# Kernel tuning notes

Hardware: AMD Instinct MI355X
Metric: run time of the kernel (lower is better)

## Reference

```python
import jax, jax.numpy as jnp
import numpy as np

EPS = 1e-15

def gcn_sparse(x, row, col, ew, W, b, n):
    # PyG GCNConv: h = x@W; add self-loops (weight 1); sym-normalize; aggregate at col (target); + bias
    h = x @ W
    loop = jnp.arange(n)
    r = jnp.concatenate([row, loop])
    c = jnp.concatenate([col, loop])
    w = jnp.concatenate([ew, jnp.ones((n,), x.dtype)])
    deg = jax.ops.segment_sum(w, c, num_segments=n)
    dinv = jnp.where(deg > 0, deg ** -0.5, 0.0)
    norm = dinv[r] * w * dinv[c]
    out = jax.ops.segment_sum(norm[:, None] * h[r], c, num_segments=n)
    return out + b

def gcn_dense(x, adj, W, b):
    # Dense equivalent of dense_to_sparse + GCNConv: existing nonzero self-loops keep their
    # weight, zero-diagonal nodes get a self-loop of weight 1 (add_remaining_self_loops).
    diag = jnp.diagonal(adj)
    adj_h = adj + jnp.diag(jnp.where(diag == 0, 1.0, 0.0).astype(adj.dtype))
    deg = adj_h.sum(axis=0)  # degree at target (col) nodes
    dinv = jnp.where(deg > 0, deg ** -0.5, 0.0)
    a_norm = dinv[:, None] * adj_h * dinv[None, :]  # norm_ij = d_i^-1/2 a_ij d_j^-1/2
    return a_norm.T @ (x @ W) + b  # out_j = sum_i norm_ij h_i

def diff_pool(x, adj, s, mask=None):
    s = jax.nn.softmax(s, axis=-1)
    if mask is not None:
        x = x * mask[:, None]
        s = s * mask[:, None]
    out = s.T @ x                      # [C, F]
    out_adj = s.T @ (adj @ s)          # [C, C]
    link = jnp.linalg.norm(adj - s @ s.T) / adj.size
    ent = jnp.mean(jnp.sum(-s * jnp.log(s + EPS), axis=-1))
    return out, out_adj, link, ent

def setup_inputs() -> dict:
    N, E, F, H, C1, C2, NC = 8192, 262144, 128, 128, 1024, 128, 16
    key = jax.random.key(0)
    ks = jax.random.split(key, 16)
    x0 = jax.random.normal(ks[0], (N, F), dtype=jnp.float32)
    edge_index = jax.random.randint(ks[1], (2, E), 0, N, dtype=jnp.int32)
    edge_weight = jax.random.uniform(ks[2], (E,), dtype=jnp.float32)
    adj = jnp.zeros((N, N), jnp.float32).at[edge_index[0], edge_index[1]].add(edge_weight)
    mask = jnp.ones((N,), jnp.float32)
    g = lambda k, i, o: jax.random.normal(k, (i, o), dtype=jnp.float32) * (1.0 / np.sqrt(i))
    return {
        'x0': x0, 'edge_index': edge_index, 'edge_weight': edge_weight,
        'adj': adj, 'mask': mask,
        'W0_in': g(ks[3], F, H),      'b0_in': jnp.zeros((H,)),
        'Wp1':   g(ks[4], H, C1),     'bp1':   jnp.zeros((C1,)),
        'W1_in': g(ks[5], H, H),      'b1_in': jnp.zeros((H,)),
        'Wp2':   g(ks[6], H, C2),     'bp2':   jnp.zeros((C2,)),
        'W2_in': g(ks[7], H, H),      'b2_in': jnp.zeros((H,)),
        'W1_out': g(ks[8], 2 * H, H), 'b1_out': jnp.zeros((H,)),
        'W0_out': g(ks[9], 2 * H, NC), 'b0_out': jnp.zeros((NC,)),
    }

def reference(x0, edge_index, edge_weight, adj, mask,
              W0_in, b0_in, Wp1, bp1, W1_in, b1_in, Wp2, bp2,
              W2_in, b2_in, W1_out, b1_out, W0_out, b0_out):
    n = x0.shape[0]
    row, col = edge_index[0], edge_index[1]
    x0_ = jax.nn.relu(gcn_sparse(x0, row, col, edge_weight, W0_in, b0_in, n))
    s1 = jax.nn.relu(gcn_sparse(x0_, row, col, edge_weight, Wp1, bp1, n))
    x1, adj1, l1, e1 = diff_pool(x0_, adj, s1, mask)
    x1_ = jax.nn.relu(gcn_dense(x1, adj1, W1_in, b1_in))
    s2 = jax.nn.relu(gcn_dense(x1_, adj1, Wp2, bp2))
    x2, adj2, l2, e2 = diff_pool(x1_, adj1, s2)
    x2_out = jax.nn.relu(gcn_dense(x2, adj2, W2_in, b2_in))
    x2_out_up = s2 @ x2_out  # unpool with pre-softmax relu s2, as in source
    x1_out = jax.nn.relu(gcn_dense(jnp.concatenate([x1_, x2_out_up], axis=1), adj1, W1_out, b1_out))
    x1_out_up = s1 @ x1_out
    x0_out = jax.nn.relu(gcn_sparse(jnp.concatenate([x0_, x1_out_up], axis=1), row, col, edge_weight, W0_out, b0_out, n))
    prediction = jax.nn.log_softmax(x0_out, axis=1)
    edge_loss = l1 + e1 + l2 + e2
    return prediction, s1, edge_loss, adj1
```

## Files before the change

### kernel.cpp

```cpp
#include <hip/hip_runtime.h>
#include <math.h>


#define N_NODES 8192
#define N_EDGES 262144

typedef __attribute__((ext_vector_type(8))) short short8;
typedef __attribute__((ext_vector_type(4))) float floatx4;

#define OFF_DEG     0
#define OFF_CNTC    8192
#define OFF_CNTR    16384
#define OFF_SCAL    24576
#define ZERO_FLOATS 24592
#define OFF_COLPTR  24592
#define OFF_ROWPTR  32785
#define OFF_CURC    40978
#define OFF_CURR    49170
#define OFF_COLR    57362
#define OFF_COLN    319506
#define OFF_ROWC    581650
#define OFF_ROWW    843794
#define OFF_DINV    1105938
#define OFF_X0      1114144
#define OFF_H0      2162720
#define OFF_S       3211296
#define OFF_AN1TB   OFF_S
#define OFF_ADJ1B   (OFF_S+524288)
#define OFF_HAT     (OFF_S+1048576)
#define OFF_HBT     (OFF_S+1114112)
#define OFF_HCATT   (OFF_S+1179648)
#define OFF_S2ST    (OFF_S+1245184)
#define OFF_X0T     7405600
#define OFF_X0B     7929888
#define A2          8454176
#define OFF_X1      (A2+0)
#define OFF_Y16     (A2+131072)
#define OFF_X1_     (A2+262144)
#define OFF_S2      (A2+524288)
#define OFF_S2S     (A2+655360)
#define OFF_U       (A2+786432)
#define OFF_X2      (A2+917504)
#define OFF_ADJ2    (A2+933888)
#define OFF_HC      (A2+950272)
#define OFF_X2_     (A2+966656)
#define OFF_Z2      (A2+999424)
#define OFF_P16     (A2+1392640)
#define OFF_DEG1    OFF_P16
#define OFF_DIAGV   (OFF_P16+1024)
#define OFF_DI2     (A2+1656832)
#define OFF_DF2     (A2+1656960)
#define OFF_ST      10111264
#define OFF_TBF     14305568
#define OFF_WP1T    OFF_TBF
#define OFF_PT      OFF_TBF
#define OFF_S1B     22694176
#define OFF_TT2     32131360

#define OUT_PRED 0
#define OUT_S1   131072
#define OUT_LOSS 8519680
#define OUT_ADJ1 8519681

__device__ __forceinline__ unsigned short f2bf(float f) {
    union { float f; unsigned u; } v; v.f = f;
    unsigned r = (v.u + 0x7FFF + ((v.u >> 16) & 1)) >> 16;
    return (unsigned short)r;
}
__device__ __forceinline__ float bf2f(unsigned short b) {
    union { unsigned u; float f; } v; v.u = (unsigned)b << 16; return v.f;
}
__device__ __forceinline__ void gl_lds16(const unsigned short* g, unsigned short* l) {
    __builtin_amdgcn_global_load_lds(
        (const __attribute__((address_space(1))) void*)g,
        (__attribute__((address_space(3))) void*)l, 16, 0, 0);
}


__global__ __launch_bounds__(256) void k_hist_gemm(
        const int* __restrict__ row, const int* __restrict__ col,
        const float* __restrict__ ew, int E,
        float* deg, int* cntc, int* cntr, float* sumA2,
        const float* __restrict__ A, const float* __restrict__ B,
        unsigned short* __restrict__ C) {
    __shared__ float As[16][68];
    __shared__ float Bs[16][68];
    int tid = threadIdx.x;
    if (blockIdx.x < 1024) {
        float* red = &As[0][0];
        int e = blockIdx.x * 256 + tid;
        float w2 = 0.f;
        if (e < E) {
            int r = row[e], c = col[e];
            float w = ew[e];
            atomicAdd(&deg[c], w);
            atomicAdd(&cntc[c], 1);
            atomicAdd(&cntr[r], 1);
            w2 = w * w;
        }
        red[tid] = w2; __syncthreads();
        for (int s = 128; s > 0; s >>= 1) { if (tid < s) red[tid] += red[tid + s]; __syncthreads(); }
        if (tid == 0) atomicAdd(sumA2, red[0]);
        return;
    }
    int bidx = blockIdx.x - 1024;
    int tx = tid & 15, ty = tid >> 4;
    int m0 = (bidx >> 1) * 64, n0 = (bidx & 1) * 64;
    const int M = 8192, N = 128, K = 128;
    float acc[4][4] = {};
    for (int k0 = 0; k0 < K; k0 += 16) {
        for (int l = 0; l < 4; ++l) {
            int idx = tid + 256 * l;
            int mm = idx >> 4, kk = idx & 15;
            As[kk][mm] = A[(size_t)(m0 + mm) * K + k0 + kk];
            int kk2 = idx >> 6, nn = idx & 63;
            Bs[kk2][nn] = B[(size_t)(k0 + kk2) * N + n0 + nn];
        }
        __syncthreads();
        #pragma unroll
        for (int kk = 0; kk < 16; ++kk) {
            float a[4], b[4];
            #pragma unroll
            for (int i = 0; i < 4; ++i) a[i] = As[kk][ty * 4 + i];
            #pragma unroll
            for (int j = 0; j < 4; ++j) b[j] = Bs[kk][tx * 4 + j];
            #pragma unroll
            for (int i = 0; i < 4; ++i)
                #pragma unroll
                for (int j = 0; j < 4; ++j) acc[i][j] += a[i] * b[j];
        }
        __syncthreads();
    }
    for (int i = 0; i < 4; ++i)
        for (int j = 0; j < 4; ++j)
            C[(size_t)(m0 + ty * 4 + i) * N + n0 + tx * 4 + j] = f2bf(acc[i][j]);
    (void)M;
}

__global__ __launch_bounds__(1024) void k_scan(const int* cntc, const int* cntr,
        int* colptr, int* rowptr, int* curc, int* curr, int n, int E,
        const float* __restrict__ deg, float* __restrict__ dinv) {
    __shared__ int part[1024];
    int tid = threadIdx.x;
    const int per = 8;
    for (int pass = 0; pass < 2; ++pass) {
        const int* cnt = pass ? cntr : cntc;
        int* ptr = pass ? rowptr : colptr;
        int* cur = pass ? curr : curc;
        int st = tid * per;
        int loc[per]; int s = 0;
        for (int i = 0; i < per; ++i) { loc[i] = s; s += cnt[st + i]; }
        part[tid] = s; __syncthreads();
        for (int off = 1; off < 1024; off <<= 1) {
            int v = part[tid];
            int add = (tid >= off) ? part[tid - off] : 0;
            __syncthreads();
            part[tid] = v + add;
            __syncthreads();
        }
        int pre = (tid == 0) ? 0 : part[tid - 1];
        for (int i = 0; i < per; ++i) { int v = pre + loc[i]; ptr[st + i] = v; cur[st + i] = v; }
        if (tid == 0) ptr[n] = E;
        __syncthreads();
    }
    for (int i = tid; i < n; i += 1024) {
        float d = deg[i] + 1.0f;
        dinv[i] = (d > 0.f) ? 1.0f / sqrtf(d) : 0.f;
    }
}

__global__ void k_scatter(const int* __restrict__ row, const int* __restrict__ col,
                          const float* __restrict__ ew, int E, const float* __restrict__ dinv,
                          int* curc, int* curr, int* colr, float* coln, int* rowc, float* roww) {
    int e = blockIdx.x * 256 + threadIdx.x;
    if (e >= E) return;
    int r = row[e], c = col[e];
    float w = ew[e];
    float nrm = dinv[r] * w * dinv[c];
    int p = atomicAdd(&curc[c], 1);
    colr[p] = r; coln[p] = nrm;
    int q = atomicAdd(&curr[r], 1);
    rowc[q] = c; roww[q] = w;
}


__global__ __launch_bounds__(256) void gemm_ab32(const float* __restrict__ A, const float* __restrict__ B,
        float* __restrict__ C, int M, int N, int K,
        const float* __restrict__ bias, int relu, int accum) {
    __shared__ float As[32][33];
    __shared__ float Bs[32][33];
    int tid = threadIdx.x, tx = tid & 15, ty = tid >> 4;
    int m0 = blockIdx.y * 32, n0 = blockIdx.x * 32;
    float acc[2][2] = {};
    for (int k0 = 0; k0 < K; k0 += 32) {
        #pragma unroll
        for (int l = 0; l < 4; ++l) {
            int idx = tid + 256 * l;
            int r = idx >> 5, c = idx & 31;
            As[r][c] = A[(size_t)(m0 + r) * K + k0 + c];
            Bs[r][c] = B[(size_t)(k0 + r) * N + n0 + c];
        }
        __syncthreads();
        #pragma unroll
        for (int kk = 0; kk < 32; ++kk) {
            float a0 = As[ty * 2][kk], a1 = As[ty * 2 + 1][kk];
            float b0 = Bs[kk][tx * 2], b1 = Bs[kk][tx * 2 + 1];
            acc[0][0] += a0 * b0; acc[0][1] += a0 * b1;
            acc[1][0] += a1 * b0; acc[1][1] += a1 * b1;
        }
        __syncthreads();
    }
    #pragma unroll
    for (int i = 0; i < 2; ++i)
        #pragma unroll
        for (int j = 0; j < 2; ++j) {
            int m = m0 + ty * 2 + i, n = n0 + tx * 2 + j;
            float v = acc[i][j];
            if (accum) v += C[(size_t)m * N + n];
            if (bias) v += bias[n];
// ... 7 lines not shown
    __shared__ float As[32][33];
    __shared__ float Bs[32][33];
    int tid = threadIdx.x, tx = tid & 15, ty = tid >> 4;
    int m0 = blockIdx.y * 32, n0 = blockIdx.x * 32;
    float acc[2][2] = {};
    for (int k0 = 0; k0 < K; k0 += 32) {
        #pragma unroll
        for (int l = 0; l < 4; ++l) {
            int idx = tid + 256 * l;
            int r = idx >> 5, c = idx & 31;
            As[r][c] = A[(size_t)(m0 + r) * K + k0 + c];
            Bs[r][c] = B[(size_t)(k0 + r) * N + n0 + c];
        }
        __syncthreads();
        #pragma unroll
        for (int kk = 0; kk < 32; ++kk) {
            float a0 = As[ty * 2][kk], a1 = As[ty * 2 + 1][kk];
            float b0 = Bs[kk][tx * 2], b1 = Bs[kk][tx * 2 + 1];
            acc[0][0] += a0 * b0; acc[0][1] += a0 * b1;
            acc[1][0] += a1 * b0; acc[1][1] += a1 * b1;
        }
        __syncthreads();
    }
    #pragma unroll
    for (int i = 0; i < 2; ++i)
        #pragma unroll
        for (int j = 0; j < 2; ++j)
            As[ty * 2 + i][tx * 2 + j] = acc[i][j];
    __syncthreads();
    int nl = tid >> 3, moff = (tid & 7) * 4;
    ushort4 o;
    o.x = f2bf(As[moff + 0][nl]);
    o.y = f2bf(As[moff + 1][nl]);
    o.z = f2bf(As[moff + 2][nl]);
    o.w = f2bf(As[moff + 3][nl]);
    *(ushort4*)(CT + (size_t)(n0 + nl) * M + m0 + moff) = o;
}

__global__ __launch_bounds__(256) void gemm_dual_bt(const float* __restrict__ A0,
        const float* __restrict__ B0, const float* __restrict__ A1, const float* __restrict__ B1,
        unsigned short* __restrict__ CT, int M, int N, int Kc) {
    __shared__ float As[32][33];
    __shared__ float Bs[32][33];
    int tid = threadIdx.x, tx = tid & 15, ty = tid >> 4;
    int m0 = blockIdx.y * 32, n0 = blockIdx.x * 32;
    float acc[2][2] = {};
    for (int src = 0; src < 2; ++src) {
        const float* A = src ? A1 : A0;
        const float* B = src ? B1 : B0;
        for (int k0 = 0; k0 < Kc; k0 += 32) {
            #pragma unroll
            for (int l = 0; l < 4; ++l) {
                int idx = tid + 256 * l;
                int r = idx >> 5, c = idx & 31;
                As[r][c] = A[(size_t)(m0 + r) * Kc + k0 + c];
                Bs[r][c] = B[(size_t)(k0 + r) * N + n0 + c];
            }
            __syncthreads();
            #pragma unroll
            for (int kk = 0; kk < 32; ++kk) {
                float a0 = As[ty * 2][kk], a1 = As[ty * 2 + 1][kk];
                float b0 = Bs[kk][tx * 2], b1 = Bs[kk][tx * 2 + 1];
                acc[0][0] += a0 * b0; acc[0][1] += a0 * b1;
                acc[1][0] += a1 * b0; acc[1][1] += a1 * b1;
            }
            __syncthreads();
        }
    }
    #pragma unroll
    for (int i = 0; i < 2; ++i)
        #pragma unroll
        for (int j = 0; j < 2; ++j)
            As[ty * 2 + i][tx * 2 + j] = acc[i][j];
    __syncthreads();
    int nl = tid >> 3, moff = (tid & 7) * 4;
    ushort4 o;
    o.x = f2bf(As[moff + 0][nl]);
    o.y = f2bf(As[moff + 1][nl]);
    o.z = f2bf(As[moff + 2][nl]);
    o.w = f2bf(As[moff + 3][nl]);
    *(ushort4*)(CT + (size_t)(n0 + nl) * M + m0 + moff) = o;
}

__global__ __launch_bounds__(256) void gemm_atb32n(const float* __restrict__ A, const float* __restrict__ B,
        float* __restrict__ C, int M, int N, int K,
        const float* __restrict__ bias, const float* __restrict__ kscale,
        const float* __restrict__ dfixv, const float* __restrict__ mscale) {
    __shared__ float As[32][33];
    __shared__ float Bs[32][33];
    int tid = threadIdx.x, tx = tid & 15, ty = tid >> 4;
    int m0 = blockIdx.y * 32, n0 = blockIdx.x * 32;
    float acc[2][2] = {};
    for (int k0 = 0; k0 < K; k0 += 32) {
        #pragma unroll
        for (int l = 0; l < 4; ++l) {
            int idx = tid + 256 * l;
            int r = idx >> 5, c = idx & 31;
            int k = k0 + r, m = m0 + c;
            float v = A[(size_t)k * M + m];
            if (k == m) v += dfixv[m];
            As[c][r] = v * kscale[k];
            Bs[r][c] = B[(size_t)k * N + n0 + c];
        }
        __syncthreads();
        #pragma unroll
        for (int kk = 0; kk < 32; ++kk) {
            float a0 = As[ty * 2][kk], a1 = As[ty * 2 + 1][kk];
            float b0 = Bs[kk][tx * 2], b1 = Bs[kk][tx * 2 + 1];
            acc[0][0] += a0 * b0; acc[0][1] += a0 * b1;
            acc[1][0] += a1 * b0; acc[1][1] += a1 * b1;
        }
        __syncthreads();
    }
    #pragma unroll
    for (int i = 0; i < 2; ++i)
        #pragma unroll
        for (int j = 0; j < 2; ++j) {
            int m = m0 + ty * 2 + i, n = n0 + tx * 2 + j;
            float v = acc[i][j] * mscale[m] + bias[n];
            C[(size_t)m * N + n] = fmaxf(v, 0.f);
        }
}

__global__ __launch_bounds__(256) void k_atb32_3(const float* __restrict__ A,
        const float* __restrict__ B0, const float* __restrict__ B1, const float* __restrict__ B2,
        float* __restrict__ C0, float* __restrict__ C1, float* ss_acc,
        int M, int N, int K) {
    __shared__ float As[32][33];
    __shared__ float Bs[32][33];
    __shared__ float red[256];
    int op = blockIdx.z;
    const float* B = (op == 0) ? B0 : (op == 1) ? B1 : B2;
    int tid = threadIdx.x, tx = tid & 15, ty = tid >> 4;
    int m0 = blockIdx.y * 32, n0 = blockIdx.x * 32;
    float acc[2][2] = {};
    for (int k0 = 0; k0 < K; k0 += 32) {
        #pragma unroll
        for (int l = 0; l < 4; ++l) {
            int idx = tid + 256 * l;
            int r = idx >> 5, c = idx & 31;
            As[c][r] = A[(size_t)(k0 + r) * M + m0 + c];
            Bs[r][c] = B[(size_t)(k0 + r) * N + n0 + c];
        }
        __syncthreads();
        #pragma unroll
        for (int kk = 0; kk < 32; ++kk) {
            float a0 = As[ty * 2][kk], a1 = As[ty * 2 + 1][kk];
            float b0 = Bs[kk][tx * 2], b1 = Bs[kk][tx * 2 + 1];
            acc[0][0] += a0 * b0; acc[0][1] += a0 * b1;
            acc[1][0] += a1 * b0; acc[1][1] += a1 * b1;
        }
        __syncthreads();
    }
    if (op == 2) {
        float ss = acc[0][0] * acc[0][0] + acc[0][1] * acc[0][1]
                 + acc[1][0] * acc[1][0] + acc[1][1] * acc[1][1];
        red[tid] = ss; __syncthreads();
        for (int s = 128; s > 0; s >>= 1) { if (tid < s) red[tid] += red[tid + s]; __syncthreads(); }
        if (tid == 0) atomicAdd(ss_acc, red[0]);
        return;
    }
    float* C = (op == 0) ? C0 : C1;
    #pragma unroll
    for (int i = 0; i < 2; ++i)
        #pragma unroll
        for (int j = 0; j < 2; ++j)
            C[(size_t)(m0 + ty * 2 + i) * N + n0 + tx * 2 + j] = acc[i][j];
}

__global__ __launch_bounds__(256) void k_hC_coldfix(
        const float* __restrict__ x2, const float* __restrict__ W2,
        float* __restrict__ hC, const float* __restrict__ adj2,
        float* di2, float* df2, float* cross2_out) {
    if (blockIdx.z == 0) {
        __shared__ float As[32][33];
        __shared__ float Bs[32][33];
        int tid = threadIdx.x, tx = tid & 15, ty = tid >> 4;
        int m0 = blockIdx.y * 32, n0 = blockIdx.x * 32;
        float acc[2][2] = {};
        for (int k0 = 0; k0 < 128; k0 += 32) {
            #pragma unroll
            for (int l = 0; l < 4; ++l) {
                int idx = tid + 256 * l;
                int r = idx >> 5, c = idx & 31;
                As[r][c] = x2[(size_t)(m0 + r) * 128 + k0 + c];
                Bs[r][c] = W2[(size_t)(k0 + r) * 128 + n0 + c];
            }
            __syncthreads();
            #pragma unroll
            for (int kk = 0; kk < 32; ++kk) {
                float a0 = As[ty * 2][kk], a1 = As[ty * 2 + 1][kk];
                float b0 = Bs[kk][tx * 2], b1 = Bs[kk][tx * 2 + 1];
                acc[0][0] += a0 * b0; acc[0][1] += a0 * b1;
                acc[1][0] += a1 * b0; acc[1][1] += a1 * b1;
            }
            __syncthreads();
        }
        #pragma unroll
        for (int i = 0; i < 2; ++i)
            #pragma unroll
            for (int j = 0; j < 2; ++j)
                hC[(size_t)(m0 + ty * 2 + i) * 128 + n0 + tx * 2 + j] = acc[i][j];
    } else {
        if (blockIdx.x | blockIdx.y) return;
        __shared__ float red[256];
        int tid = threadIdx.x;
        float diag = 0.f;
        if (tid < 128) {
            float s = 0.f;
            for (int i = 0; i < 128; ++i) s += adj2[(size_t)i * 128 + tid];
            diag = adj2[(size_t)tid * 128 + tid];
            float fix = (diag == 0.f) ? 1.0f : 0.f;
            s += fix;
            df2[tid] = fix;
            di2[tid] = (s > 0.f) ? 1.0f / sqrtf(s) : 0.f;
        }
        red[tid] = diag; __syncthreads();
        for (int st = 128; st > 0; st >>= 1) { if (tid < st) red[tid] += red[tid + st]; __syncthreads(); }
        if (tid == 0) *cross2_out = red[0];
    }
}


__global__ __launch_bounds__(256) void gemm_tn_bf16_tiles(
        const unsigned short* __restrict__ ST_,
        const unsigned short* __restrict__ TT_,
        const unsigned short* __restrict__ X0T_,
        float* __restrict__ P, int K) {
    __shared__ __align__(16) unsigned short As[128 * 64];
    __shared__ __align__(16) unsigned short Bs[128 * 64];
    int tid = threadIdx.x;
    int wave = tid >> 6, lane = tid & 63;
    int wm = wave >> 1, wn = wave & 1;
    int lin = blockIdx.x + gridDim.x * blockIdx.y;
    int p432 = (lin & 7) * 54 + (lin >> 3);
    int f = p432 >> 2, z = p432 & 3;
    int m = 0, Pfx = 0;
    while (f >= Pfx + 17 - m) { Pfx += 17 - m; ++m; }
    int r = f - Pfx;
    int t, n0; const unsigned short* B;
    if (r < 8)           { t = m * 8 + r;                                n0 = r * 128;    B = TT_; }
    else if (r < 16 - m) { int tj = m + (r - 8);
                           t = 64 + (8 * m - m * (m - 1) / 2) + (r - 8); n0 = tj * 128;   B = ST_; }
    else                 { t = 100 + m;                                  n0 = 0;          B = X0T_; }
    int m0 = m * 128;
    int kchunk = K >> 2;
    int k0 = z * kchunk;
    float* Pz = P + ((size_t)z * 108 + t) * 16384;
    floatx4 acc[4][4] = {};
    int q = lane >> 4, lm = lane & 15;
    int lrow = lane >> 3, lcol = (lane & 7) * 8;
    for (int kt = 0; kt < kchunk; kt += 64) {
        int gk0 = k0 + kt;
        #pragma unroll
        for (int p = 0; p < 4; ++p) {
            int rbase = wave * 32 + p * 8;
            int rrow = rbase + lrow;
            int scol = lcol ^ ((rrow & 7) * 8);
            gl_lds16(&ST_[(size_t)(m0 + rrow) * K + gk0 + scol], &As[rbase * 64]);
            gl_lds16(&B[(size_t)(n0 + rrow) * K + gk0 + scol], &Bs[rbase * 64]);
        }
        __syncthreads();
        #pragma unroll
        for (int ks = 0; ks < 64; ks += 32) {
            short8 af[4], bf[4];
            int kk = ks + q * 8;
            #pragma unroll
            for (int i = 0; i < 4; ++i) {
                int ml = wm * 64 + i * 16 + lm;
                af[i] = *(const short8*)(&As[ml * 64 + (kk ^ ((ml & 7) * 8))]);
                int nl = wn * 64 + i * 16 + lm;
                bf[i] = *(const short8*)(&Bs[nl * 64 + (kk ^ ((nl & 7) * 8))]);
            }
            #pragma unroll
            for (int i = 0; i < 4; ++i)
                #pragma unroll
                for (int j = 0; j < 4; ++j)
                    acc[i][j] = __builtin_amdgcn_mfma_f32_16x16x32_bf16(af[i], bf[j], acc[i][j], 0, 0, 0);
        }
        __syncthreads();
    }
    for (int i = 0; i < 4; ++i) {
        int lr = wm * 64 + i * 16 + q * 4;
        for (int j = 0; j < 4; ++j) {
            int lc = wn * 64 + j * 16 + lm;
            #pragma unroll
            for (int rr = 0; rr < 4; ++rr)
                Pz[(size_t)(lr + rr) * 128 + lc] = acc[i][j][rr];
        }
    }
}

__global__ __launch_bounds__(256) void k_reduce_tiles(
        const float* __restrict__ P,
        float* __restrict__ adj1o, unsigned short* __restrict__ adj1b,
        float* __restrict__ x1, float* __restrict__ deg1, float* __restrict__ diagv,
        float* __restrict__ scal) {
    __shared__ float colsum[128];
    __shared__ float red[256];
    int tile = blockIdx.y, half = blockIdx.x, tid = threadIdx.x;
    if (tid < 128) colsum[tid] = 0.f;
    __syncthreads();
    int m, n, kind;
// ... 187 lines not shown
    }
}

__global__ __launch_bounds__(256) void k_gemm16_mfma(
        const unsigned short* __restrict__ A0,
        const unsigned short* __restrict__ A1,
        const float* __restrict__ B0,
        const float* __restrict__ B1,
        float* __restrict__ C) {
    __shared__ __align__(16) unsigned short As[128 * 64];
    __shared__ __align__(16) unsigned short Bs[16 * 64];
    int tid = threadIdx.x, wave = tid >> 6, lane = tid & 63;
    int m0 = blockIdx.x * 128;
    int q = lane >> 4, lm = lane & 15;
    int lrow = lane >> 3, lcol = (lane & 7) * 8;
    floatx4 acc[2] = {};
    for (int seg = 0; seg < 2; ++seg) {
        const unsigned short* A = seg ? A1 : A0;
        const float* Bsrc = seg ? B1 : B0;
        int Ks = seg ? 1024 : 128;
        for (int kt = 0; kt < Ks; kt += 64) {
            #pragma unroll
            for (int p = 0; p < 4; ++p) {
                int rbase = wave * 32 + p * 8;
                int row = rbase + lrow;
                int scol = lcol ^ ((row & 7) * 8);
                gl_lds16(&A[(size_t)(m0 + row) * Ks + kt + scol], &As[rbase * 64]);
            }
            for (int e = tid; e < 1024; e += 256) {
                int n = e >> 6, kk = e & 63;
                Bs[n * 64 + (kk ^ ((n & 7) * 8))] = f2bf(Bsrc[(size_t)(kt + kk) * 16 + n]);
            }
            __syncthreads();
            #pragma unroll
            for (int ks = 0; ks < 64; ks += 32) {
                int kk = ks + q * 8;
                short8 bf = *(const short8*)(&Bs[lm * 64 + (kk ^ ((lm & 7) * 8))]);
                #pragma unroll
                for (int i = 0; i < 2; ++i) {
                    int ml = wave * 32 + i * 16 + lm;
                    short8 af = *(const short8*)(&As[ml * 64 + (kk ^ ((ml & 7) * 8))]);
                    acc[i] = __builtin_amdgcn_mfma_f32_16x16x32_bf16(af, bf, acc[i], 0, 0, 0);
                }
            }
            __syncthreads();
        }
    }
    #pragma unroll
    for (int i = 0; i < 2; ++i) {
        int rowb = m0 + wave * 32 + i * 16 + q * 4;
        #pragma unroll
        for (int r = 0; r < 4; ++r)
            C[(size_t)(rowb + r) * 16 + lm] = acc[i][r];
    }
}


__device__ __forceinline__ void f2b_body(float* tile ,
        const float* __restrict__ in, unsigned short* __restrict__ outb,
        int R, int C, const float* __restrict__ rowscale, int bx, int by, int t) {
    int rb = by * 64, cb = bx * 64;
    int lr = t >> 4, lc4 = (t & 15) * 4;
    #pragma unroll
    for (int p = 0; p < 4; ++p) {
        int r = rb + lr + p * 16;
        float4 v = *(const float4*)(in + (size_t)r * C + cb + lc4);
        float s = rowscale ? rowscale[r] : 1.0f;
        tile[(lr + p * 16) * 65 + lc4 + 0] = v.x * s;
        tile[(lr + p * 16) * 65 + lc4 + 1] = v.y * s;
        tile[(lr + p * 16) * 65 + lc4 + 2] = v.z * s;
        tile[(lr + p * 16) * 65 + lc4 + 3] = v.w * s;
    }
    __syncthreads();
    int cc0 = t >> 5, rr = (t & 31) * 2;
    #pragma unroll
    for (int p = 0; p < 8; ++p) {
        int cc = cc0 + p * 8;
        unsigned a = f2bf(tile[rr * 65 + cc]);
        unsigned b = f2bf(tile[(rr + 1) * 65 + cc]);
        *(unsigned*)(outb + (size_t)(cb + cc) * R + rb + rr) = a | (b << 16);
    }
}

__global__ __launch_bounds__(256) void k_f2b2(
        const float* __restrict__ in0, unsigned short* __restrict__ out0,
        const float* __restrict__ in1, unsigned short* __restrict__ out1,
        const float* __restrict__ mask) {
    __shared__ float tile[64 * 65];
    int b = blockIdx.x, t = threadIdx.x;
    if (b < 32) f2b_body(tile, in0, out0, 128, 1024, nullptr, b & 15, b >> 4, t);
    else { int bb = b - 32; f2b_body(tile, in1, out1, 8192, 128, mask, bb & 1, bb >> 1, t); }
}

__global__ __launch_bounds__(256) void k_transpose_b2b2(
        const unsigned short* __restrict__ in0, unsigned short* __restrict__ out0,
        const unsigned short* __restrict__ in1, unsigned short* __restrict__ out1,
        int R, int C) {
    __shared__ __align__(16) unsigned short tile[64][72];
    const unsigned short* in = blockIdx.z ? in1 : in0;
    unsigned short* out = blockIdx.z ? out1 : out0;
    int rb = blockIdx.y * 64, cb = blockIdx.x * 64;
    int t = threadIdx.x;
    int lr = t >> 3, lc = (t & 7) * 8;
    #pragma unroll
    for (int p = 0; p < 2; ++p) {
        int r = lr + p * 32;
        *(short8*)(&tile[r][lc]) = *(const short8*)(&in[(size_t)(rb + r) * C + cb + lc]);
    }
    __syncthreads();
    int cc0 = t >> 4, rr = (t & 15) * 4;
    #pragma unroll
    for (int p = 0; p < 4; ++p) {
        int cc = cc0 + p * 16;
        unsigned long long v = (unsigned long long)tile[rr][cc]
                             | ((unsigned long long)tile[rr + 1][cc] << 16)
                             | ((unsigned long long)tile[rr + 2][cc] << 32)
                             | ((unsigned long long)tile[rr + 3][cc] << 48);
        *(unsigned long long*)(&out[(size_t)(cb + cc) * R + rb + rr]) = v;
    }
}

__global__ __launch_bounds__(256) void k_anorm_hat(const float* __restrict__ adjm,
        const float* __restrict__ deg1, const float* __restrict__ diagv,
        unsigned short* __restrict__ outb,
        const float* __restrict__ Ax1, const float* __restrict__ BW1,
        unsigned short* __restrict__ HATo) {
    __shared__ float sm[64 * 65 + 192];
    int t = threadIdx.x;
    if (blockIdx.x < 256) {
        const int n = 1024;
        float* tile = sm;
        float* drow = sm + 4160;
        float* frow = sm + 4224;
        float* dcol = sm + 4288;
        int rb = (blockIdx.x >> 4) * 64, cb = (blockIdx.x & 15) * 64;
        if (t < 64) {
            int i = rb + t;
            float fi = (diagv[i] == 0.f) ? 1.0f : 0.f;
            float s = deg1[i] + fi;
            frow[t] = fi;
            drow[t] = (s > 0.f) ? 1.0f / sqrtf(s) : 0.f;
        } else if (t < 128) {
            int j = cb + (t - 64);
            float fj = (diagv[j] == 0.f) ? 1.0f : 0.f;
            float s = deg1[j] + fj;
            dcol[t - 64] = (s > 0.f) ? 1.0f / sqrtf(s) : 0.f;
        }
        __syncthreads();
        int lr = t >> 4, lc4 = (t & 15) * 4;
        #pragma unroll
        for (int p = 0; p < 4; ++p) {
            int rl = lr + p * 16;
            int i = rb + rl;
            float4 v = *(const float4*)(adjm + (size_t)i * n + cb + lc4);
            float di = drow[rl];
            float vv[4] = {v.x, v.y, v.z, v.w};
            #pragma unroll
            for (int qq = 0; qq < 4; ++qq) {
                int j = cb + lc4 + qq;
                float val = vv[qq];
                if (i == j) val += frow[rl];
                tile[rl * 65 + lc4 + qq] = di * val * dcol[lc4 + qq];
            }
        }
        __syncthreads();
        int cc0 = t >> 5, rr = (t & 31) * 2;
        #pragma unroll
        for (int p = 0; p < 8; ++p) {
            int cc = cc0 + p * 8;
            unsigned a = f2bf(tile[rr * 65 + cc]);
            unsigned b = f2bf(tile[(rr + 1) * 65 + cc]);
            *(unsigned*)(outb + (size_t)(cb + cc) * n + rb + rr) = a | (b << 16);
        }
        return;
// ... 205 lines not shown
    for (int q = 0; q < 8; ++q)
        ow[q] = (unsigned)f2bf(a[q * 2]) | ((unsigned)f2bf(a[q * 2 + 1]) << 16);
    uint4* outp = (uint4*)(tb + (size_t)r * 1024 + j0);
    outp[0] = make_uint4(ow[0], ow[1], ow[2], ow[3]);
    outp[1] = make_uint4(ow[4], ow[5], ow[6], ow[7]);
}


extern "C" void kernel_launch(void* const* d_in, const int* in_sizes, int n_in,
                              void* d_out, int out_size, void* d_ws, size_t ws_size,
                              hipStream_t stream) {
    const int N = N_NODES, E = N_EDGES;
    const float* x0     = (const float*)d_in[0];
    const int*   eidx   = (const int*)d_in[1];
    const float* ew     = (const float*)d_in[2];
    const float* mask   = (const float*)d_in[4];
    const float* W0_in  = (const float*)d_in[5];
    const float* b0_in  = (const float*)d_in[6];
    const float* Wp1    = (const float*)d_in[7];
    const float* bp1    = (const float*)d_in[8];
    const float* W1_in  = (const float*)d_in[9];
    const float* b1_in  = (const float*)d_in[10];
    const float* Wp2    = (const float*)d_in[11];
    const float* bp2    = (const float*)d_in[12];
    const float* W2_in  = (const float*)d_in[13];
    const float* b2_in  = (const float*)d_in[14];
    const float* W1_out = (const float*)d_in[15];
    const float* b1_out = (const float*)d_in[16];
    const float* W0_out = (const float*)d_in[17];
    const float* b0_out = (const float*)d_in[18];

    float* out   = (float*)d_out;
    float* predo = out + OUT_PRED;
    float* s1o   = out + OUT_S1;
    float* losso = out + OUT_LOSS;
    float* adj1o = out + OUT_ADJ1;

    float* wsf = (float*)d_ws;
    int*   wsi = (int*)d_ws;
    float* deg   = wsf + OFF_DEG;
    int*   cntc  = wsi + OFF_CNTC;
    int*   cntr  = wsi + OFF_CNTR;
    float* scal  = wsf + OFF_SCAL;
    int*   cptr  = wsi + OFF_COLPTR;
    int*   rptr  = wsi + OFF_ROWPTR;
    int*   curc  = wsi + OFF_CURC;
    int*   curr  = wsi + OFF_CURR;
    int*   colr  = wsi + OFF_COLR;
    float* coln  = wsf + OFF_COLN;
    int*   rowc  = wsi + OFF_ROWC;
    float* roww  = wsf + OFF_ROWW;
    float* dinv  = wsf + OFF_DINV;
    float* x0_   = wsf + OFF_X0;
    unsigned short* h0b   = (unsigned short*)(wsf + OFF_H0);
    unsigned short* Sb    = (unsigned short*)(wsf + OFF_S);
    unsigned short* TT    = (unsigned short*)(wsf + OFF_TT2);
    unsigned short* AN1TB = (unsigned short*)(wsf + OFF_AN1TB);
    unsigned short* ADJ1B = (unsigned short*)(wsf + OFF_ADJ1B);
    unsigned short* HAT   = (unsigned short*)(wsf + OFF_HAT);
    unsigned short* HBT   = (unsigned short*)(wsf + OFF_HBT);
    unsigned short* HCATT = (unsigned short*)(wsf + OFF_HCATT);
    unsigned short* S2ST  = (unsigned short*)(wsf + OFF_S2ST);
    unsigned short* ST    = (unsigned short*)(wsf + OFF_ST);
    unsigned short* TBF   = (unsigned short*)(wsf + OFF_TBF);
    unsigned short* WP1T  = (unsigned short*)(wsf + OFF_WP1T);
    unsigned short* X0T   = (unsigned short*)(wsf + OFF_X0T);
    unsigned short* x0b   = (unsigned short*)(wsf + OFF_X0B);
    unsigned short* s1b   = (unsigned short*)(wsf + OFF_S1B);
    float* PT    = wsf + OFF_PT;
    float* x1    = wsf + OFF_X1;
    float* y16   = wsf + OFF_Y16;
    float* x1_   = wsf + OFF_X1_;
    float* s2    = wsf + OFF_S2;
    float* S2s   = wsf + OFF_S2S;
    float* u     = wsf + OFF_U;
    float* x2    = wsf + OFF_X2;
    float* adj2  = wsf + OFF_ADJ2;
    float* hC    = wsf + OFF_HC;
    float* x2_   = wsf + OFF_X2_;
    float* z2    = wsf + OFF_Z2;
    float* p16   = wsf + OFF_P16;
    float* deg1  = wsf + OFF_DEG1;
    float* diagv = wsf + OFF_DIAGV;
    float* di2   = wsf + OFF_DI2;
    float* df2   = wsf + OFF_DF2;

    const int* row = eidx;
    const int* col = eidx + E;

    hipMemsetAsync(wsf, 0, (size_t)ZERO_FLOATS * sizeof(float), stream);
    hipMemsetAsync(deg1, 0, 1024 * sizeof(float), stream);
    hipMemsetAsync(y16, 0, 1024 * 16 * sizeof(float), stream);

    k_hist_gemm<<<1280, 256, 0, stream>>>(row, col, ew, E, deg, cntc, cntr, &scal[3],
                                          x0, W0_in, h0b);
    k_scan<<<1, 1024, 0, stream>>>(cntc, cntr, cptr, rptr, curc, curr, N, E, deg, dinv);
    k_scatter<<<E / 256, 256, 0, stream>>>(row, col, ew, E, dinv, curc, curr, colr, coln, rowc, roww);

    k_agg_b16<<<N, 64, 0, stream>>>(h0b, x0_, x0b, cptr, colr, coln, dinv, b0_in, 1);

    k_agg_b16<<<N, 64, 0, stream>>>(x0b, nullptr, h0b, cptr, colr, coln, dinv, nullptr, 0);
    k_f2b2<<<288, 256, 0, stream>>>(Wp1, WP1T, x0_, X0T, mask);
    gemm_tn_bf16_store<<<dim3(64, 8), 256, 0, stream>>>(h0b, WP1T, s1o, s1b, 8192, 1024, 128, bp1, 1);

    k_softmax1024<<<N, 256, 0, stream>>>(s1o, Sb, mask, &scal[0]);
    k_spmm_seg<<<N / 4, 256, 0, stream>>>(Sb, rptr, rowc, roww, TBF);
    k_transpose_b2b2<<<dim3(16, 128, 2), 256, 0, stream>>>(Sb, ST, TBF, TT, 8192, 1024);

    gemm_tn_bf16_tiles<<<dim3(108, 4), 256, 0, stream>>>(ST, TT, X0T, PT, 8192);
    k_reduce_tiles<<<dim3(2, 108), 256, 0, stream>>>(PT, adj1o, ADJ1B, x1, deg1, diagv, scal);
    k_anorm_hat<<<384, 256, 0, stream>>>(adj1o, deg1, diagv, AN1TB, x1, W1_in, HAT);

    gemm_tn_bf16_n128<<<dim3(16, 2), 256, 0, stream>>>(AN1TB, HAT, x1_, 1024, b1_in, 1, nullptr, nullptr);
    gemm_ab32_bt<<<dim3(4, 32), 256, 0, stream>>>(x1_, Wp2, HBT, 1024, 128, 128);
    gemm_tn_bf16_n128<<<dim3(16, 2), 256, 0, stream>>>(AN1TB, HBT, s2, 1024, bp2, 1, nullptr, nullptr);

    k_softmax128_t<<<1024, 128, 0, stream>>>(s2, S2s, S2ST, &scal[5]);
    gemm_tn_bf16_n128<<<dim3(16, 2), 256, 0, stream>>>(ADJ1B, S2ST, u, 1024, nullptr, 0, nullptr, nullptr);
    k_atb32_3<<<dim3(4, 4, 3), 256, 0, stream>>>(S2s, x1_, u, S2s, x2, adj2, &scal[7], 128, 128, 1024);

    k_hC_coldfix<<<dim3(4, 4, 2), 256, 0, stream>>>(x2, W2_in, hC, adj2, di2, df2, &scal[6]);
    gemm_atb32n<<<dim3(4, 4), 256, 0, stream>>>(adj2, hC, x2_, 128, 128, 128, b2_in, di2, df2, di2);

    gemm_ab32<<<dim3(4, 4), 256, 0, stream>>>(x2_, W1_out + 128 * 128, z2, 128, 128, 128, nullptr, 0, 0);
    gemm_dual_bt<<<dim3(4, 32), 256, 0, stream>>>(x1_, W1_out, s2, z2, HCATT, 1024, 128, 128);
    gemm_tn_bf16_n128<<<dim3(16, 2), 256, 0, stream>>>(AN1TB, HCATT, nullptr, 1024, b1_out, 1,
                                                       W0_out + 128 * 16, y16);

    k_gemm16_mfma<<<64, 256, 0, stream>>>(x0b, s1b, W0_out, y16, p16);
    k_agg16_ls<<<512, 256, 0, stream>>>(p16, predo, cptr, colr, coln, dinv, b0_out, scal, losso);
}
```

Baseline: 889.1 us.

## Fuse small pool-2 GEMMs and merge second aggregation with bf16 conversions

Rebuilds the second diff-pool stage's kernel chain. The u = adj1·S2 MFMA GEMM now runs alongside x2 and the S2ᵀS2 sum-of-squares in one launch. adj2 and hC share a second launch, and the adj2 column-degree/diag fix is computed redundantly per block inside the final normalized GEMM, removing one launch and the di2/df2 buffers. Separately, the second sparse aggregation is rewritten with 4 nodes per 256-thread block and 4-way edge unrolling, and it absorbs the Wp1/x0_ bf16 transpose-conversion kernel. The aim is fewer launches and better occupancy, at the cost of duplicated degree computation across 16 blocks.

```diff
diff --git a/kernel.cpp b/kernel.cpp
--- a/kernel.cpp
+++ b/kernel.cpp
@@ -48,8 +48,6 @@
 #define OFF_P16     (A2+1392640)
 #define OFF_DEG1    OFF_P16
 #define OFF_DIAGV   (OFF_P16+1024)
-#define OFF_DI2     (A2+1656832)
-#define OFF_DF2     (A2+1656960)
 #define OFF_ST      10111264
 #define OFF_TBF     14305568
 #define OFF_WP1T    OFF_TBF
@@ -106,7 +104,7 @@
     int bidx = blockIdx.x - 1024;
     int tx = tid & 15, ty = tid >> 4;
     int m0 = (bidx >> 1) * 64, n0 = (bidx & 1) * 64;
-    const int M = 8192, N = 128, K = 128;
+    const int N = 128, K = 128;
     float acc[4][4] = {};
     for (int k0 = 0; k0 < K; k0 += 16) {
         for (int l = 0; l < 4; ++l) {
@@ -134,7 +132,6 @@
     for (int i = 0; i < 4; ++i)
         for (int j = 0; j < 4; ++j)
             C[(size_t)(m0 + ty * 4 + i) * N + n0 + tx * 4 + j] = f2bf(acc[i][j]);
-    (void)M;
 }
 
 __global__ __launch_bounds__(1024) void k_scan(const int* cntc, const int* cntr,
@@ -308,31 +305,201 @@
     *(ushort4*)(CT + (size_t)(n0 + nl) * M + m0 + moff) = o;
 }
 
-__global__ __launch_bounds__(256) void gemm_atb32n(const float* __restrict__ A, const float* __restrict__ B,
-        float* __restrict__ C, int M, int N, int K,
-        const float* __restrict__ bias, const float* __restrict__ kscale,
-        const float* __restrict__ dfixv, const float* __restrict__ mscale) {
-    __shared__ float As[32][33];
-    __shared__ float Bs[32][33];
-    int tid = threadIdx.x, tx = tid & 15, ty = tid >> 4;
-    int m0 = blockIdx.y * 32, n0 = blockIdx.x * 32;
+__global__ __launch_bounds__(256) void k_u_x2(
+        const unsigned short* __restrict__ ADJ1B, const unsigned short* __restrict__ S2ST,
+        float* __restrict__ u,
+        const float* __restrict__ S2s, const float* __restrict__ x1_,
+        float* __restrict__ x2, float* ss_acc) {
+    __shared__ __align__(16) unsigned short As[64 * 64];
+    __shared__ __align__(16) unsigned short Bs[64 * 64];
+    __shared__ float fS[2112];
+    __shared__ float red[256];
+    int bid = blockIdx.x, t = threadIdx.x;
+    if (bid < 32) {
+        int wave = t >> 6, lane = t & 63;
+        int m0 = (bid & 15) * 64, n0 = (bid >> 4) * 64;
+        floatx4 acc[4] = {};
+        int q = lane >> 4, lm = lane & 15;
+        int lrow = lane >> 3, lcol = (lane & 7) * 8;
+        for (int kt = 0; kt < 1024; kt += 64) {
+            #pragma unroll
+            for (int p = 0; p < 2; ++p) {
+                int rbase = wave * 16 + p * 8;
+                int row = rbase + lrow;
+                int scol = lcol ^ ((row & 7) * 8);
+                gl_lds16(&ADJ1B[(size_t)(m0 + row) * 1024 + kt + scol], &As[rbase * 64]);
+                gl_lds16(&S2ST[(size_t)(n0 + row) * 1024 + kt + scol], &Bs[rbase * 64]);
+            }
+            __syncthreads();
+            #pragma unroll
+            for (int ks = 0; ks < 64; ks += 32) {
+                int kk = ks + q * 8;
+                int ml = wave * 16 + lm;
+                short8 af = *(const short8*)(&As[ml * 64 + (kk ^ ((ml & 7) * 8))]);
+                #pragma unroll
+                for (int j = 0; j < 4; ++j) {
+                    int nl = j * 16 + lm;
+                    short8 bf = *(const short8*)(&Bs[nl * 64 + (kk ^ ((nl & 7) * 8))]);
+                    acc[j] = __builtin_amdgcn_mfma_f32_16x16x32_bf16(af, bf, acc[j], 0, 0, 0);
+                }
+            }
+            __syncthreads();
+        }
+        #pragma unroll
+        for (int j = 0; j < 4; ++j) {
+            int col = n0 + j * 16 + lm;
+            int rowb = m0 + wave * 16 + q * 4;
+            #pragma unroll
+            for (int r = 0; r < 4; ++r)
+                u[(size_t)(rowb + r) * 128 + col] = acc[j][r];
+        }
+        return;
+    }
+    int op = (bid - 32) >> 4, rem = (bid - 32) & 15;
+    const float* B = op ? S2s : x1_;
+    float* fA = fS; float* fB = fS + 1056;
+    int tx = t & 15, ty = t >> 4;
+    int m0 = (rem >> 2) * 32, n0 = (rem & 3) * 32;
+    float acc2[2][2] = {};
+    for (int k0 = 0; k0 < 1024; k0 += 32) {
+        #pragma unroll
+        for (int l = 0; l < 4; ++l) {
+            int idx = t + 256 * l;
+            int r = idx >> 5, c = idx & 31;
+            fA[c * 33 + r] = S2s[(size_t)(k0 + r) * 128 + m0 + c];
+            fB[r * 33 + c] = B[(size_t)(k0 + r) * 128 + n0 + c];
+        }
+        __syncthreads();
+        #pragma unroll
+        for (int kk = 0; kk < 32; ++kk) {
+            float a0 = fA[(ty * 2) * 33 + kk], a1 = fA[(ty * 2 + 1) * 33 + kk];
+            float b0 = fB[kk * 33 + tx * 2], b1 = fB[kk * 33 + tx * 2 + 1];
+            acc2[0][0] += a0 * b0; acc2[0][1] += a0 * b1;
+            acc2[1][0] += a1 * b0; acc2[1][1] += a1 * b1;
+        }
+        __syncthreads();
+    }
+    if (op == 1) {
+        float ss = acc2[0][0] * acc2[0][0] + acc2[0][1] * acc2[0][1]
+                 + acc2[1][0] * acc2[1][0] + acc2[1][1] * acc2[1][1];
+        red[t] = ss; __syncthreads();
+        for (int s = 128; s > 0; s >>= 1) { if (t < s) red[t] += red[t + s]; __syncthreads(); }
+        if (t == 0) atomicAdd(ss_acc, red[0]);
+        return;
+    }
+    #pragma unroll
+    for (int i = 0; i < 2; ++i)
+        #pragma unroll
+        for (int j = 0; j < 2; ++j)
+            x2[(size_t)(m0 + ty * 2 + i) * 128 + n0 + tx * 2 + j] = acc2[i][j];
+}
+
+__global__ __launch_bounds__(256) void k_adj2_hC(
+        const float* __restrict__ S2s, const float* __restrict__ u, float* __restrict__ adj2,
+        const float* __restrict__ x2, const float* __restrict__ W2, float* __restrict__ hC) {
+    __shared__ float fS[2112];
+    int bid = blockIdx.x, t = threadIdx.x;
+    float* fA = fS; float* fB = fS + 1056;
+    int tx = t & 15, ty = t >> 4;
+    if (bid < 16) {
+        int m0 = (bid >> 2) * 32, n0 = (bid & 3) * 32;
+        float acc[2][2] = {};
+        for (int k0 = 0; k0 < 1024; k0 += 32) {
+            #pragma unroll
+            for (int l = 0; l < 4; ++l) {
+                int idx = t + 256 * l;
+                int r = idx >> 5, c = idx & 31;
+                fA[c * 33 + r] = S2s[(size_t)(k0 + r) * 128 + m0 + c];
+                fB[r * 33 + c] = u[(size_t)(k0 + r) * 128 + n0 + c];
+            }
+            __syncthreads();
+            #pragma unroll
+            for (int kk = 0; kk < 32; ++kk) {
+                float a0 = fA[(ty * 2) * 33 + kk], a1 = fA[(ty * 2 + 1) * 33 + kk];
+                float b0 = fB[kk * 33 + tx * 2], b1 = fB[kk * 33 + tx * 2 + 1];
+                acc[0][0] += a0 * b0; acc[0][1] += a0 * b1;
+                acc[1][0] += a1 * b0; acc[1][1] += a1 * b1;
+            }
+            __syncthreads();
+        }
+        #pragma unroll
+        for (int i = 0; i < 2; ++i)
+            #pragma unroll
+            for (int j = 0; j < 2; ++j)
+                adj2[(size_t)(m0 + ty * 2 + i) * 128 + n0 + tx * 2 + j] = acc[i][j];
+    } else {
+        int bb = bid - 16;
+        int m0 = (bb >> 2) * 32, n0 = (bb & 3) * 32;
+        float acc[2][2] = {};
+        for (int k0 = 0; k0 < 128; k0 += 32) {
+            #pragma unroll
+            for (int l = 0; l < 4; ++l) {
+                int idx = t + 256 * l;
+                int r = idx >> 5, c = idx & 31;
+                fA[r * 33 + c] = x2[(size_t)(m0 + r) * 128 + k0 + c];
+                fB[r * 33 + c] = W2[(size_t)(k0 + r) * 128 + n0 + c];
+            }
+            __syncthreads();
+            #pragma unroll
+            for (int kk = 0; kk < 32; ++kk) {
+                float a0 = fA[(ty * 2) * 33 + kk], a1 = fA[(ty * 2 + 1) * 33 + kk];
+                float b0 = fB[kk * 33 + tx * 2], b1 = fB[kk * 33 + tx * 2 + 1];
+                acc[0][0] += a0 * b0; acc[0][1] += a0 * b1;
+                acc[1][0] += a1 * b0; acc[1][1] += a1 * b1;
+            }
+            __syncthreads();
+        }
+        #pragma unroll
+        for (int i = 0; i < 2; ++i)
+            #pragma unroll
+            for (int j = 0; j < 2; ++j)
+                hC[(size_t)(m0 + ty * 2 + i) * 128 + n0 + tx * 2 + j] = acc[i][j];
+    }
+}
+
+__global__ __launch_bounds__(256) void k_atb32n_cf(
+        const float* __restrict__ adj2, const float* __restrict__ hC,
+        float* __restrict__ x2_, const float* __restrict__ bias, float* cross2_out) {
+    __shared__ float fS[2112];
+    __shared__ float sdi[128], sdf[128];
+    __shared__ float red[256];
+    int t = threadIdx.x;
+    float diag = 0.f;
+    if (t < 128) {
+        float s = 0.f;
+        for (int i = 0; i < 128; ++i) s += adj2[(size_t)i * 128 + t];
+        diag = adj2[(size_t)t * 128 + t];
+        float fix = (diag == 0.f) ? 1.0f : 0.f;
+        s += fix;
+        sdf[t] = fix;
+        sdi[t] = (s > 0.f) ? 1.0f / sqrtf(s) : 0.f;
+    }
+    if (blockIdx.x == 0) {
+        red[t] = (t < 128) ? diag : 0.f; __syncthreads();
+        for (int st = 128; st > 0; st >>= 1) { if (t < st) red[t] += red[t + st]; __syncthreads(); }
+        if (t == 0) *cross2_out = red[0];
+    }
+    __syncthreads();
+    float* fA = fS; float* fB = fS + 1056;
+    int tx = t & 15, ty = t >> 4;
+    int m0 = ((int)blockIdx.x >> 2) * 32, n0 = ((int)blockIdx.x & 3) * 32;
     float acc[2][2] = {};
-    for (int k0 = 0; k0 < K; k0 += 32) {
+    for (int k0 = 0; k0 < 128; k0 += 32) {
         #pragma unroll
         for (int l = 0; l < 4; ++l) {
-            int idx = tid + 256 * l;
+            int idx = t + 256 * l;
             int r = idx >> 5, c = idx & 31;
             int k = k0 + r, m = m0 + c;
-            float v = A[(size_t)k * M + m];
-            if (k == m) v += dfixv[m];
-            As[c][r] = v * kscale[k];
-            Bs[r][c] = B[(size_t)k * N + n0 + c];
+            float v = adj2[(size_t)k * 128 + m];
+            if (k == m) v += sdf[m];
+            fA[c * 33 + r] = v * sdi[k];
+            fB[r * 33 + c] = hC[(size_t)k * 128 + n0 + c];
         }
         __syncthreads();
         #pragma unroll
         for (int kk = 0; kk < 32; ++kk) {
-            float a0 = As[ty * 2][kk], a1 = As[ty * 2 + 1][kk];
-            float b0 = Bs[kk][tx * 2], b1 = Bs[kk][tx * 2 + 1];
+            float a0 = fA[(ty * 2) * 33 + kk], a1 = fA[(ty * 2 + 1) * 33 + kk];
+            float b0 = fB[kk * 33 + tx * 2], b1 = fB[kk * 33 + tx * 2 + 1];
             acc[0][0] += a0 * b0; acc[0][1] += a0 * b1;
             acc[1][0] += a1 * b0; acc[1][1] += a1 * b1;
         }
@@ -343,108 +510,9 @@
         #pragma unroll
         for (int j = 0; j < 2; ++j) {
             int m = m0 + ty * 2 + i, n = n0 + tx * 2 + j;
-            float v = acc[i][j] * mscale[m] + bias[n];
-            C[(size_t)m * N + n] = fmaxf(v, 0.f);
-        }
-}
-
-__global__ __launch_bounds__(256) void k_atb32_3(const float* __restrict__ A,
-        const float* __restrict__ B0, const float* __restrict__ B1, const float* __restrict__ B2,
-        float* __restrict__ C0, float* __restrict__ C1, float* ss_acc,
-        int M, int N, int K) {
-    __shared__ float As[32][33];
-    __shared__ float Bs[32][33];
-    __shared__ float red[256];
-    int op = blockIdx.z;
-    const float* B = (op == 0) ? B0 : (op == 1) ? B1 : B2;
-    int tid = threadIdx.x, tx = tid & 15, ty = tid >> 4;
-    int m0 = blockIdx.y * 32, n0 = blockIdx.x * 32;
-    float acc[2][2] = {};
-    for (int k0 = 0; k0 < K; k0 += 32) {
-        #pragma unroll
-        for (int l = 0; l < 4; ++l) {
-            int idx = tid + 256 * l;
-            int r = idx >> 5, c = idx & 31;
-            As[c][r] = A[(size_t)(k0 + r) * M + m0 + c];
-            Bs[r][c] = B[(size_t)(k0 + r) * N + n0 + c];
-        }
-        __syncthreads();
-        #pragma unroll
-        for (int kk = 0; kk < 32; ++kk) {
-            float a0 = As[ty * 2][kk], a1 = As[ty * 2 + 1][kk];
-            float b0 = Bs[kk][tx * 2], b1 = Bs[kk][tx * 2 + 1];
-            acc[0][0] += a0 * b0; acc[0][1] += a0 * b1;
-            acc[1][0] += a1 * b0; acc[1][1] += a1 * b1;
-        }
-        __syncthreads();
-    }
-    if (op == 2) {
-        float ss = acc[0][0] * acc[0][0] + acc[0][1] * acc[0][1]
-                 + acc[1][0] * acc[1][0] + acc[1][1] * acc[1][1];
-        red[tid] = ss; __syncthreads();
-        for (int s = 128; s > 0; s >>= 1) { if (tid < s) red[tid] += red[tid + s]; __syncthreads(); }
-        if (tid == 0) atomicAdd(ss_acc, red[0]);
-        return;
-    }
-    float* C = (op == 0) ? C0 : C1;
-    #pragma unroll
-    for (int i = 0; i < 2; ++i)
-        #pragma unroll
-        for (int j = 0; j < 2; ++j)
-            C[(size_t)(m0 + ty * 2 + i) * N + n0 + tx * 2 + j] = acc[i][j];
-}
-
-__global__ __launch_bounds__(256) void k_hC_coldfix(
-        const float* __restrict__ x2, const float* __restrict__ W2,
-        float* __restrict__ hC, const float* __restrict__ adj2,
-        float* di2, float* df2, float* cross2_out) {
-    if (blockIdx.z == 0) {
-        __shared__ float As[32][33];
-        __shared__ float Bs[32][33];
-        int tid = threadIdx.x, tx = tid & 15, ty = tid >> 4;
-        int m0 = blockIdx.y * 32, n0 = blockIdx.x * 32;
-        float acc[2][2] = {};
-        for (int k0 = 0; k0 < 128; k0 += 32) {
-            #pragma unroll
-            for (int l = 0; l < 4; ++l) {
-                int idx = tid + 256 * l;
-                int r = idx >> 5, c = idx & 31;
-                As[r][c] = x2[(size_t)(m0 + r) * 128 + k0 + c];
-                Bs[r][c] = W2[(size_t)(k0 + r) * 128 + n0 + c];
-            }
-            __syncthreads();
-            #pragma unroll
-            for (int kk = 0; kk < 32; ++kk) {
-                float a0 = As[ty * 2][kk], a1 = As[ty * 2 + 1][kk];
-                float b0 = Bs[kk][tx * 2], b1 = Bs[kk][tx * 2 + 1];
-                acc[0][0] += a0 * b0; acc[0][1] += a0 * b1;
-                acc[1][0] += a1 * b0; acc[1][1] += a1 * b1;
-            }
-            __syncthreads();
-        }
-        #pragma unroll
-        for (int i = 0; i < 2; ++i)
-            #pragma unroll
-            for (int j = 0; j < 2; ++j)
-                hC[(size_t)(m0 + ty * 2 + i) * 128 + n0 + tx * 2 + j] = acc[i][j];
-    } else {
-        if (blockIdx.x | blockIdx.y) return;
-        __shared__ float red[256];
-        int tid = threadIdx.x;
-        float diag = 0.f;
-        if (tid < 128) {
-            float s = 0.f;
-            for (int i = 0; i < 128; ++i) s += adj2[(size_t)i * 128 + tid];
-            diag = adj2[(size_t)tid * 128 + tid];
-            float fix = (diag == 0.f) ? 1.0f : 0.f;
-            s += fix;
-            df2[tid] = fix;
-            di2[tid] = (s > 0.f) ? 1.0f / sqrtf(s) : 0.f;
-        }
-        red[tid] = diag; __syncthreads();
-        for (int st = 128; st > 0; st >>= 1) { if (tid < st) red[tid] += red[tid + st]; __syncthreads(); }
-        if (tid == 0) *cross2_out = red[0];
-    }
+            float v = acc[i][j] * sdi[m] + bias[n];
+            x2_[(size_t)m * 128 + n] = fmaxf(v, 0.f);
+        }
 }
 
 
@@ -798,14 +866,51 @@
     }
 }
 
-__global__ __launch_bounds__(256) void k_f2b2(
-        const float* __restrict__ in0, unsigned short* __restrict__ out0,
-        const float* __restrict__ in1, unsigned short* __restrict__ out1,
+__global__ __launch_bounds__(256) void k_agg_f2b(
+        const unsigned short* __restrict__ h, unsigned short* __restrict__ outb,
+        const int* __restrict__ cptr, const int* __restrict__ colr,
+        const float* __restrict__ coln, const float* __restrict__ dinv,
+        const float* __restrict__ Wp1, unsigned short* __restrict__ WP1T,
+        const float* __restrict__ x0_, unsigned short* __restrict__ X0T,
         const float* __restrict__ mask) {
     __shared__ float tile[64 * 65];
     int b = blockIdx.x, t = threadIdx.x;
-    if (b < 32) f2b_body(tile, in0, out0, 128, 1024, nullptr, b & 15, b >> 4, t);
-    else { int bb = b - 32; f2b_body(tile, in1, out1, 8192, 128, mask, bb & 1, bb >> 1, t); }
+    if (b >= 2048) {
+        int bb = b - 2048;
+        if (bb < 32) f2b_body(tile, Wp1, WP1T, 128, 1024, nullptr, bb & 15, bb >> 4, t);
+        else { bb -= 32; f2b_body(tile, x0_, X0T, 8192, 128, mask, bb & 1, bb >> 1, t); }
+        return;
+    }
+    int c = b * 4 + (t >> 6);
+    int lane = t & 63;
+    int f0 = lane * 2;
+    float d = dinv[c], dd = d * d;
+    const unsigned short* hf = h + f0;
+    unsigned uu = *(const unsigned*)(hf + (size_t)c * 128);
+    float a0 = dd * bf2f((unsigned short)(uu & 0xffff));
+    float a1 = dd * bf2f((unsigned short)(uu >> 16));
+    int e0 = cptr[c], e1 = cptr[c + 1];
+    int e = e0;
+    for (; e + 4 <= e1; e += 4) {
+        int r0 = colr[e], r1 = colr[e + 1], r2 = colr[e + 2], r3 = colr[e + 3];
+        float w0 = coln[e], w1 = coln[e + 1], w2 = coln[e + 2], w3 = coln[e + 3];
+        unsigned v0 = *(const unsigned*)(hf + (size_t)r0 * 128);
+        unsigned v1 = *(const unsigned*)(hf + (size_t)r1 * 128);
+        unsigned v2 = *(const unsigned*)(hf + (size_t)r2 * 128);
+        unsigned v3 = *(const unsigned*)(hf + (size_t)r3 * 128);
+        a0 += w0 * bf2f((unsigned short)(v0 & 0xffff)) + w1 * bf2f((unsigned short)(v1 & 0xffff))
+            + w2 * bf2f((unsigned short)(v2 & 0xffff)) + w3 * bf2f((unsigned short)(v3 & 0xffff));
+        a1 += w0 * bf2f((unsigned short)(v0 >> 16)) + w1 * bf2f((unsigned short)(v1 >> 16))
+            + w2 * bf2f((unsigned short)(v2 >> 16)) + w3 * bf2f((unsigned short)(v3 >> 16));
+    }
+    for (; e < e1; ++e) {
+        float w = coln[e];
+        unsigned v = *(const unsigned*)(hf + (size_t)colr[e] * 128);
+        a0 += w * bf2f((unsigned short)(v & 0xffff));
+        a1 += w * bf2f((unsigned short)(v >> 16));
+    }
+    unsigned o = (unsigned)f2bf(a0) | ((unsigned)f2bf(a1) << 16);
+    *(unsigned*)(outb + (size_t)c * 128 + f0) = o;
 }
 
 __global__ __launch_bounds__(256) void k_transpose_b2b2(
@@ -1177,8 +1282,6 @@
     float* p16   = wsf + OFF_P16;
     float* deg1  = wsf + OFF_DEG1;
     float* diagv = wsf + OFF_DIAGV;
-    float* di2   = wsf + OFF_DI2;
-    float* df2   = wsf + OFF_DF2;
 
     const int* row = eidx;
     const int* col = eidx + E;
@@ -1194,8 +1297,8 @@
 
     k_agg_b16<<<N, 64, 0, stream>>>(h0b, x0_, x0b, cptr, colr, coln, dinv, b0_in, 1);
 
-    k_agg_b16<<<N, 64, 0, stream>>>(x0b, nullptr, h0b, cptr, colr, coln, dinv, nullptr, 0);
-    k_f2b2<<<288, 256, 0, stream>>>(Wp1, WP1T, x0_, X0T, mask);
+    k_agg_f2b<<<2336, 256, 0, stream>>>(x0b, h0b, cptr, colr, coln, dinv,
+                                        Wp1, WP1T, x0_, X0T, mask);
     gemm_tn_bf16_store<<<dim3(64, 8), 256, 0, stream>>>(h0b, WP1T, s1o, s1b, 8192, 1024, 128, bp1, 1);
 
     k_softmax1024<<<N, 256, 0, stream>>>(s1o, Sb, mask, &scal[0]);
@@ -1211,11 +1314,9 @@
     gemm_tn_bf16_n128<<<dim3(16, 2), 256, 0, stream>>>(AN1TB, HBT, s2, 1024, bp2, 1, nullptr, nullptr);
 
     k_softmax128_t<<<1024, 128, 0, stream>>>(s2, S2s, S2ST, &scal[5]);
-    gemm_tn_bf16_n128<<<dim3(16, 2), 256, 0, stream>>>(ADJ1B, S2ST, u, 1024, nullptr, 0, nullptr, nullptr);
-    k_atb32_3<<<dim3(4, 4, 3), 256, 0, stream>>>(S2s, x1_, u, S2s, x2, adj2, &scal[7], 128, 128, 1024);
-
-    k_hC_coldfix<<<dim3(4, 4, 2), 256, 0, stream>>>(x2, W2_in, hC, adj2, di2, df2, &scal[6]);
-    gemm_atb32n<<<dim3(4, 4), 256, 0, stream>>>(adj2, hC, x2_, 128, 128, 128, b2_in, di2, df2, di2);
+    k_u_x2<<<64, 256, 0, stream>>>(ADJ1B, S2ST, u, S2s, x1_, x2, &scal[7]);
+    k_adj2_hC<<<32, 256, 0, stream>>>(S2s, u, adj2, x2, W2_in, hC);
+    k_atb32n_cf<<<16, 256, 0, stream>>>(adj2, hC, x2_, b2_in, &scal[6]);
 
     gemm_ab32<<<dim3(4, 4), 256, 0, stream>>>(x2_, W1_out + 128 * 128, z2, 128, 128, 128, nullptr, 0, 0);
     gemm_dual_bt<<<dim3(4, 32), 256, 0, stream>>>(x1_, W1_out, s2, z2, HCATT, 1024, 128, 128);
```

Measured after the change: 893.1 us. No clear change (+0.4%).
